# Performance work log

Hardware: AMD Instinct MI355X
Metric: run time of the kernel (lower is better)

The kernel has to match this reference:

```python
import jax, jax.numpy as jnp
import numpy as np

B, T, D, H = 4, 2048, 1024, 16


def setup_inputs() -> dict:
    key = jax.random.key(0)
    ks = jax.random.split(key, 5)
    s = 0.02  # keep activations sane
    return {
        "x": jax.random.normal(ks[0], (B, T, D), jnp.float32),
        "Wq": jax.random.normal(ks[1], (D, D), jnp.float32) * s,
        "bq": jnp.zeros((D,), jnp.float32),
        "Wk": jax.random.normal(ks[2], (D, D), jnp.float32) * s,
        "bk": jnp.zeros((D,), jnp.float32),
        "Wv": jax.random.normal(ks[3], (D, D), jnp.float32) * s,
        "bv": jnp.zeros((D,), jnp.float32),
        "Wo": jax.random.normal(ks[4], (D, D), jnp.float32) * s,
        "bo": jnp.zeros((D,), jnp.float32),
    }


def _split_heads(t):  # (B,T,D) -> (B,H,T,d)
    b, s, d = t.shape
    return t.reshape(b, s, H, d // H).transpose(0, 2, 1, 3)


def reference(x, Wq, bq, Wk, bk, Wv, bv, Wo, bo):
    d_k = D // H
    q = _split_heads(x @ Wq + bq)  # (B,H,T,d)
    k = _split_heads(x @ Wk + bk)
    v = _split_heads(x @ Wv + bv)
    # scaled dot-product similarities (B,H,T,T)
    scores = jnp.einsum("bhqd,bhkd->bhqk", q, k) / jnp.sqrt(jnp.asarray(d_k, x.dtype))
    # causal mask: masked_fill(tril==0, -inf)
    causal = jnp.tril(jnp.ones((T, T), bool))
    scores = jnp.where(causal, scores, -jnp.inf)
    attn = jax.nn.softmax(scores, axis=-1)
    ctx = jnp.einsum("bhqk,bhkd->bhqd", attn, v)  # (B,H,T,d)
    ctx = ctx.transpose(0, 2, 1, 3).reshape(x.shape[0], T, D)
    return ctx @ Wo + bo
```

## Files before the change

### kernel.cpp

```cpp
#include <hip/hip_runtime.h>
#include <hip/hip_bf16.h>

typedef unsigned short u16;
typedef __attribute__((ext_vector_type(8))) short bf16x8;
typedef __attribute__((ext_vector_type(4))) short bf16x4;
typedef __attribute__((ext_vector_type(4))) float f32x4;

#define DD 1024
#define TT 2048
#define HH 16
#define BB 4
#define DK 64
#define MM 8192

#define QSCALE 0.180336880f

__device__ __forceinline__ u16 f2b(float x) {
  __hip_bfloat16 h = __float2bfloat16(x);
  return *reinterpret_cast<u16*>(&h);
}

__device__ __forceinline__ unsigned pk2(float a, float b) {
  float2 t; t.x = a; t.y = b;
  __hip_bfloat162 h = __float22bfloat162_rn(t);
  union { __hip_bfloat162 h; unsigned u; } cv;
  cv.h = h;
  return cv.u;
}

#define GLD16(gp, lp)                                                         \
  __builtin_amdgcn_global_load_lds(                                           \
      (const __attribute__((address_space(1))) unsigned int*)(gp),            \
      (__attribute__((address_space(3))) unsigned int*)(lp), 16, 0, 0)

__global__ __launch_bounds__(256) void cast_bf16_kernel(
    const float* __restrict__ src, u16* __restrict__ dst, int n) {
  int i = (blockIdx.x * 256 + threadIdx.x) * 4;
  if (i + 3 < n) {
    float4 v = *reinterpret_cast<const float4*>(src + i);
    ushort4 o;
    o.x = f2b(v.x); o.y = f2b(v.y); o.z = f2b(v.z); o.w = f2b(v.w);
    *reinterpret_cast<ushort4*>(dst + i) = o;
  }
}

__global__ __launch_bounds__(256) void transpose_cast_kernel(
    const float* __restrict__ W0, const float* __restrict__ W1,
    const float* __restrict__ W2, const float* __restrict__ W3,
    u16* __restrict__ O0, u16* __restrict__ O1,
    u16* __restrict__ O2, u16* __restrict__ O3) {
  const float* W; u16* O;
  switch (blockIdx.z) {
    case 0: W = W0; O = O0; break;
    case 1: W = W1; O = O1; break;
    case 2: W = W2; O = O2; break;
    default: W = W3; O = O3; break;
  }
  __shared__ float tile[32][33];
  int tx = threadIdx.x, ty = threadIdx.y;
  int bx = blockIdx.x * 32;
  int by = blockIdx.y * 32;
#pragma unroll
  for (int j = 0; j < 4; j++)
    tile[ty + j * 8][tx] = W[(size_t)(by + ty + j * 8) * DD + bx + tx];
  __syncthreads();
#pragma unroll
  for (int j = 0; j < 4; j++)
    O[(size_t)(bx + ty + j * 8) * DD + by + tx] = f2b(tile[tx][ty + j * 8]);
}

#define GEMM_STAGE(Aptr, Bptr, Asl, Bsl)                                      \
  _Pragma("unroll") for (int c = 0; c < 4; c++) {                             \
    int idx = tid * 8 + c * 2048;                                             \
    int row = idx >> 6, ck = idx & 63;                                        \
    int src = ck ^ ((row & 7) << 3);                                          \
    GLD16(Aptr + (size_t)(m0 + row) * DD + k0 + src, Asl + idx);              \
    GLD16(Bptr + (size_t)(n0 + row) * DD + k0 + src, Bsl + idx);              \
  }

#define GEMM_MFMA(Asl, Bsl)                                                   \
  _Pragma("unroll") for (int half = 0; half < 2; half++) {                    \
    bf16x8 af[4], bfr[4];                                                     \
    _Pragma("unroll") for (int mb = 0; mb < 4; mb++) {                        \
      int r = wm + mb * 16 + l16;                                             \
      af[mb] = *reinterpret_cast<const bf16x8*>(                              \
          &Asl[r * 64 + ((half * 32 + quad * 8) ^ ((r & 7) << 3))]);          \
    }                                                                         \
    _Pragma("unroll") for (int nb = 0; nb < 4; nb++) {                        \
      int r = wn + nb * 16 + l16;                                             \
      bfr[nb] = *reinterpret_cast<const bf16x8*>(                             \
          &Bsl[r * 64 + ((half * 32 + quad * 8) ^ ((r & 7) << 3))]);          \
    }                                                                         \
    _Pragma("unroll") for (int mb = 0; mb < 4; mb++)                          \
      _Pragma("unroll") for (int nb = 0; nb < 4; nb++)                        \
          acc[mb][nb] = __builtin_amdgcn_mfma_f32_16x16x32_bf16(              \
              af[mb], bfr[nb], acc[mb][nb], 0, 0, 0);                         \
  }

__global__ __launch_bounds__(256, 4) void gemm_qkv_kernel(
    const u16* __restrict__ A,
    const u16* __restrict__ WtQ, const u16* __restrict__ WtK,
    const u16* __restrict__ WtV,
    const float* __restrict__ bq, const float* __restrict__ bk,
    const float* __restrict__ bv,
    u16* __restrict__ Qo, u16* __restrict__ Ko, u16* __restrict__ Vo) {
  __shared__ __align__(16) u16 smem[17408];
  u16* As = smem;
  u16* Bs = smem + 8192;
  u16* Vs = smem;
  int z = blockIdx.z;
  const u16* Bt = (z == 0) ? WtQ : ((z == 1) ? WtK : WtV);
  const float* bias = (z == 0) ? bq : ((z == 1) ? bk : bv);
  int tid = threadIdx.x;
  int wave = tid >> 6, lane = tid & 63;
  int quad = lane >> 4, l16 = lane & 15;
  int m0 = blockIdx.x * 128, n0 = blockIdx.y * 128;
  int wm = (wave >> 1) * 64, wn = (wave & 1) * 64;

  f32x4 acc[4][4];
#pragma unroll
  for (int i = 0; i < 4; i++)
#pragma unroll
    for (int j = 0; j < 4; j++) acc[i][j] = (f32x4){0.f, 0.f, 0.f, 0.f};

  for (int k0 = 0; k0 < DD; k0 += 64) {
    GEMM_STAGE(A, Bt, As, Bs)
    __syncthreads();
    GEMM_MFMA(As, Bs)
    __syncthreads();
  }

  if (z == 2) {
#pragma unroll
    for (int mb = 0; mb < 4; mb++)
#pragma unroll
      for (int nb = 0; nb < 4; nb++) {
        int col = wn + nb * 16 + l16;
        float bv2 = bias[n0 + col];
#pragma unroll
        for (int r = 0; r < 4; r++) {
          int row = wm + mb * 16 + quad * 4 + r;
          Vs[col * 136 + row] = f2b(acc[mb][nb][r] + bv2);
        }
      }
    __syncthreads();
    int b = m0 >> 11;
    int tloc = m0 & 2047;
#pragma unroll
    for (int i = 0; i < 8; i++) {
      int idx = tid * 8 + i * 2048;
      int row = idx >> 7, col = idx & 127;
      uint4 v = *reinterpret_cast<const uint4*>(&Vs[row * 136 + col]);
      int ncol = n0 + row, h = ncol >> 6, dd = ncol & 63;
      *reinterpret_cast<uint4*>(
          Vo + (((size_t)(b * HH + h) * DK) + dd) * TT + tloc + col) = v;
    }
    return;
  }

  u16* outp = (z == 0) ? Qo : Ko;
  float scale = (z == 0) ? QSCALE : 1.0f;
#pragma unroll
  for (int mb = 0; mb < 4; mb++) {
#pragma unroll
    for (int nb = 0; nb < 4; nb++) {
      int col = n0 + wn + nb * 16 + l16;
      float bv2 = bias[col];
#pragma unroll
      for (int r = 0; r < 4; r++) {
        int row = m0 + wm + mb * 16 + quad * 4 + r;
        float val = (acc[mb][nb][r] + bv2) * scale;
        int hh = col >> 6, dd = col & 63;
        int b = row >> 11, t = row & 2047;
        outp[(((size_t)(b * HH + hh) * TT) + t) * DK + dd] = f2b(val);
      }
    }
  }
}

__global__ __launch_bounds__(256, 4) void gemm_out_kernel(
    const u16* __restrict__ A, const u16* __restrict__ Bt,
    const float* __restrict__ bias, float* __restrict__ outp) {
  __shared__ __align__(16) u16 As[128 * 64];
  __shared__ __align__(16) u16 Bs[128 * 64];
  int tid = threadIdx.x;
  int wave = tid >> 6, lane = tid & 63;
  int quad = lane >> 4, l16 = lane & 15;
  int m0 = blockIdx.x * 128, n0 = blockIdx.y * 128;
  int wm = (wave >> 1) * 64, wn = (wave & 1) * 64;

  f32x4 acc[4][4];
#pragma unroll
  for (int i = 0; i < 4; i++)
#pragma unroll
    for (int j = 0; j < 4; j++) acc[i][j] = (f32x4){0.f, 0.f, 0.f, 0.f};

  for (int k0 = 0; k0 < DD; k0 += 64) {
    GEMM_STAGE(A, Bt, As, Bs)
    __syncthreads();
    GEMM_MFMA(As, Bs)
    __syncthreads();
  }

#pragma unroll
  for (int mb = 0; mb < 4; mb++) {
#pragma unroll
    for (int nb = 0; nb < 4; nb++) {
      int col = n0 + wn + nb * 16 + l16;
      float bv = bias[col];
#pragma unroll
      for (int r = 0; r < 4; r++) {
        int row = m0 + wm + mb * 16 + quad * 4 + r;
        outp[(size_t)row * DD + col] = acc[mb][nb][r] + bv;
      }
    }
  }
}

__global__ __launch_bounds__(512, 4) void attn_kernel(
    const u16* __restrict__ Q, const u16* __restrict__ K,
    const u16* __restrict__ VT, u16* __restrict__ ctx) {
  __shared__ __align__(16) u16 Ks[2][64][72];
  __shared__ __align__(16) u16 Vt[2][64][72];

  int tid = threadIdx.x;
  int wave = tid >> 6, lane = tid & 63;
  int quad = lane >> 4, l16 = lane & 15;
  int bid = blockIdx.x;
  int bh = bid & 63;
  int px = bid >> 6;
  int qt = px < 4 ? 15 - px : (px < 8 ? px + 4 : (px < 12 ? px - 4 : 15 - px));
  int b = bh >> 4, h = bh & 15;
  const u16* Qh = Q + (size_t)bh * TT * DK;
  const u16* Kh = K + (size_t)bh * TT * DK;
  const u16* Vh = VT + (size_t)bh * DK * TT;
  int sidx = tid * 8;

  int ktmax = 2 * qt + 1;
  int dtile = 2 * qt + (wave >> 2);
  int qrl = (wave * 16 + l16) & 63;

  const u16* qrow = Qh + (size_t)(qt * 128 + wave * 16 + l16) * DK + quad * 8;
  bf16x8 qf0 = *reinterpret_cast<const bf16x8*>(qrow);
  bf16x8 qf1 = *reinterpret_cast<const bf16x8*>(qrow + 32);

  uint4 kpre = *reinterpret_cast<const uint4*>(Kh + sidx);
  uint4 vpre = *reinterpret_cast<const uint4*>(Vh + (size_t)(sidx >> 6) * TT + (sidx & 63));
  *reinterpret_cast<uint4*>(&Ks[0][sidx >> 6][sidx & 63]) = kpre;
  *reinterpret_cast<uint4*>(&Vt[0][sidx >> 6][sidx & 63]) = vpre;
  __syncthreads();

  f32x4 oacc[4];
#pragma unroll
  for (int dt = 0; dt < 4; dt++) oacc[dt] = (f32x4){0.f, 0.f, 0.f, 0.f};
  f32x4 lacc = (f32x4){0.f, 0.f, 0.f, 0.f};
  const bf16x4 ones = (bf16x4){0x3F80, 0x3F80, 0x3F80, 0x3F80};

  for (int kt = 0; kt <= ktmax; kt++) {
    int cur = kt & 1, nxt = cur ^ 1;
    bool more = kt < ktmax;
    if (more) {
      kpre = *reinterpret_cast<const uint4*>(Kh + (size_t)(kt + 1) * 4096 + sidx);
      vpre = *reinterpret_cast<const uint4*>(
          Vh + (size_t)(sidx >> 6) * TT + (kt + 1) * 64 + (sidx & 63));
    }

    if (kt <= dtile) {
      f32x4 sacc[4];
#pragma unroll
      for (int kb = 0; kb < 4; kb++) sacc[kb] = (f32x4){0.f, 0.f, 0.f, 0.f};
#pragma unroll
      for (int kb = 0; kb < 4; kb++) {
        bf16x8 kf0 = *reinterpret_cast<const bf16x8*>(&Ks[cur][kb * 16 + l16][quad * 8]);
        bf16x8 kf1 = *reinterpret_cast<const bf16x8*>(&Ks[cur][kb * 16 + l16][32 + quad * 8]);
        sacc[kb] = __builtin_amdgcn_mfma_f32_16x16x32_bf16(kf0, qf0, sacc[kb], 0, 0, 0);
        sacc[kb] = __builtin_amdgcn_mfma_f32_16x16x32_bf16(kf1, qf1, sacc[kb], 0, 0, 0);
      }

      if (kt == dtile) {
#pragma unroll
        for (int kb = 0; kb < 4; kb++)
#pragma unroll
          for (int r = 0; r < 4; r++)
            if (kb * 16 + quad * 4 + r > qrl) sacc[kb][r] = -__builtin_inff();
      }

#pragma unroll
      for (int kb = 0; kb < 4; kb++) {
        float p0 = __builtin_amdgcn_exp2f(sacc[kb][0]);
        float p1 = __builtin_amdgcn_exp2f(sacc[kb][1]);
        float p2 = __builtin_amdgcn_exp2f(sacc[kb][2]);
        float p3 = __builtin_amdgcn_exp2f(sacc[kb][3]);
        union { unsigned u[2]; bf16x4 v; } pk;
        pk.u[0] = pk2(p0, p1);
        pk.u[1] = pk2(p2, p3);
        lacc = __builtin_amdgcn_mfma_f32_16x16x16bf16_1k(pk.v, ones, lacc, 0, 0, 0);
#pragma unroll
        for (int dt = 0; dt < 4; dt++) {
          bf16x4 vf = *reinterpret_cast<const bf16x4*>(
              &Vt[cur][dt * 16 + l16][kb * 16 + quad * 4]);
          oacc[dt] = __builtin_amdgcn_mfma_f32_16x16x16bf16_1k(pk.v, vf, oacc[dt], 0, 0, 0);
        }
      }
    }

    if (more) {
      *reinterpret_cast<uint4*>(&Ks[nxt][sidx >> 6][sidx & 63]) = kpre;
      *reinterpret_cast<uint4*>(&Vt[nxt][sidx >> 6][sidx & 63]) = vpre;
    }
    __syncthreads();
  }

  f32x4 inv;
#pragma unroll
  for (int r = 0; r < 4; r++) inv[r] = 1.0f / lacc[r];

  u16* Obuf = &Ks[0][0][0];
#pragma unroll
  for (int dt = 0; dt < 4; dt++)
#pragma unroll
    for (int r = 0; r < 4; r++)
      Obuf[(wave * 16 + quad * 4 + r) * 72 + dt * 16 + l16] =
          f2b(oacc[dt][r] * inv[r]);
  asm volatile("s_waitcnt lgkmcnt(0)" ::: "memory");
#pragma unroll
  for (int i = 0; i < 2; i++) {
    int idx = lane * 8 + i * 512;
    int row = idx >> 6, colc = idx & 63;
    uint4 v = *reinterpret_cast<const uint4*>(&Obuf[(wave * 16 + row) * 72 + colc]);
    int t = qt * 128 + wave * 16 + row;
    *reinterpret_cast<uint4*>(
        ctx + ((size_t)(b * TT + t)) * DD + h * DK + colc) = v;
  }
}

extern "C" void kernel_launch(void* const* d_in, const int* in_sizes, int n_in,
                              void* d_out, int out_size, void* d_ws, size_t ws_size,
                              hipStream_t stream) {
  const float* x  = (const float*)d_in[0];
  const float* Wq = (const float*)d_in[1];
  const float* bq = (const float*)d_in[2];
  const float* Wk = (const float*)d_in[3];
  const float* bk = (const float*)d_in[4];
  const float* Wv = (const float*)d_in[5];
  const float* bv = (const float*)d_in[6];
  const float* Wo = (const float*)d_in[7];
  const float* bo = (const float*)d_in[8];
  float* out = (float*)d_out;

  char* ws = (char*)d_ws;
  size_t off = 0;
  u16* xb  = (u16*)(ws + off); off += (size_t)MM * DD * 2;
  u16* wtq = (u16*)(ws + off); off += (size_t)DD * DD * 2;
  u16* wtk = (u16*)(ws + off); off += (size_t)DD * DD * 2;
  u16* wtv = (u16*)(ws + off); off += (size_t)DD * DD * 2;
  u16* wto = (u16*)(ws + off); off += (size_t)DD * DD * 2;
  u16* Qb  = (u16*)(ws + off); off += (size_t)MM * DD * 2;
  u16* Kb  = (u16*)(ws + off); off += (size_t)MM * DD * 2;
  u16* VTb = (u16*)(ws + off); off += (size_t)MM * DD * 2;
  u16* ctx = (u16*)(ws + off); off += (size_t)MM * DD * 2;

  {
    int n = MM * DD;
    cast_bf16_kernel<<<n / 1024, 256, 0, stream>>>(x, xb, n);
  }
  {
    dim3 grid(DD / 32, DD / 32, 4);
    dim3 block(32, 8);
    transpose_cast_kernel<<<grid, block, 0, stream>>>(Wq, Wk, Wv, Wo, wtq, wtk, wtv, wto);
  }
  {
    dim3 grid(MM / 128, DD / 128, 3);
    gemm_qkv_kernel<<<grid, 256, 0, stream>>>(xb, wtq, wtk, wtv, bq, bk, bv,
                                              Qb, Kb, VTb);
  }
  {
    attn_kernel<<<1024, 512, 0, stream>>>(Qb, Kb, VTb, ctx);
  }
  {
    dim3 grid(MM / 128, DD / 128);
    gemm_out_kernel<<<grid, 256, 0, stream>>>(ctx, wto, bo, out);
  }
}
```

Before: 237.9 us.

## Pair causal query tiles per block and widen key tiles to 128

The attention kernel now launches 512 blocks, each processing two query tiles (15-px and px) in sequence so every block does a balanced amount of causal work. Key/value tiles grow from 64 to 128 keys per iteration, halving the number of barriers and loads per query tile. On the diagonal tile each wave skips key sub-blocks above its own rows instead of computing and masking them. LDS use doubles per block and the sequential phases reduce parallelism, which may lower occupancy and latency hiding.

```diff
diff --git a/kernel.cpp b/kernel.cpp
--- a/kernel.cpp
+++ b/kernel.cpp
@@ -220,8 +220,8 @@
 __global__ __launch_bounds__(512, 4) void attn_kernel(
     const u16* __restrict__ Q, const u16* __restrict__ K,
     const u16* __restrict__ VT, u16* __restrict__ ctx) {
-  __shared__ __align__(16) u16 Ks[2][64][72];
-  __shared__ __align__(16) u16 Vt[2][64][72];
+  __shared__ __align__(16) u16 Ks[2][128][72];
+  __shared__ __align__(16) u16 Vt[2][64][136];
 
   int tid = threadIdx.x;
   int wave = tid >> 6, lane = tid & 63;
@@ -229,68 +229,67 @@
   int bid = blockIdx.x;
   int bh = bid & 63;
   int px = bid >> 6;
-  int qt = px < 4 ? 15 - px : (px < 8 ? px + 4 : (px < 12 ? px - 4 : 15 - px));
   int b = bh >> 4, h = bh & 15;
   const u16* Qh = Q + (size_t)bh * TT * DK;
   const u16* Kh = K + (size_t)bh * TT * DK;
   const u16* Vh = VT + (size_t)bh * DK * TT;
-  int sidx = tid * 8;
-
-  int ktmax = 2 * qt + 1;
-  int dtile = 2 * qt + (wave >> 2);
-  int qrl = (wave * 16 + l16) & 63;
-
-  const u16* qrow = Qh + (size_t)(qt * 128 + wave * 16 + l16) * DK + quad * 8;
-  bf16x8 qf0 = *reinterpret_cast<const bf16x8*>(qrow);
-  bf16x8 qf1 = *reinterpret_cast<const bf16x8*>(qrow + 32);
-
-  uint4 kpre = *reinterpret_cast<const uint4*>(Kh + sidx);
-  uint4 vpre = *reinterpret_cast<const uint4*>(Vh + (size_t)(sidx >> 6) * TT + (sidx & 63));
-  *reinterpret_cast<uint4*>(&Ks[0][sidx >> 6][sidx & 63]) = kpre;
-  *reinterpret_cast<uint4*>(&Vt[0][sidx >> 6][sidx & 63]) = vpre;
-  __syncthreads();
-
-  f32x4 oacc[4];
-#pragma unroll
-  for (int dt = 0; dt < 4; dt++) oacc[dt] = (f32x4){0.f, 0.f, 0.f, 0.f};
-  f32x4 lacc = (f32x4){0.f, 0.f, 0.f, 0.f};
+
+  int ki0 = tid * 8, ki1 = tid * 8 + 4096;
   const bf16x4 ones = (bf16x4){0x3F80, 0x3F80, 0x3F80, 0x3F80};
 
-  for (int kt = 0; kt <= ktmax; kt++) {
-    int cur = kt & 1, nxt = cur ^ 1;
-    bool more = kt < ktmax;
-    if (more) {
-      kpre = *reinterpret_cast<const uint4*>(Kh + (size_t)(kt + 1) * 4096 + sidx);
-      vpre = *reinterpret_cast<const uint4*>(
-          Vh + (size_t)(sidx >> 6) * TT + (kt + 1) * 64 + (sidx & 63));
-    }
-
-    if (kt <= dtile) {
-      f32x4 sacc[4];
-#pragma unroll
-      for (int kb = 0; kb < 4; kb++) sacc[kb] = (f32x4){0.f, 0.f, 0.f, 0.f};
-#pragma unroll
-      for (int kb = 0; kb < 4; kb++) {
+  for (int phase = 0; phase < 2; phase++) {
+    int qtc = phase ? px : (15 - px);
+    __syncthreads();
+
+    const u16* qrow = Qh + (size_t)(qtc * 128 + wave * 16 + l16) * DK + quad * 8;
+    bf16x8 qf0 = *reinterpret_cast<const bf16x8*>(qrow);
+    bf16x8 qf1 = *reinterpret_cast<const bf16x8*>(qrow + 32);
+
+    uint4 kp0 = *reinterpret_cast<const uint4*>(Kh + ki0);
+    uint4 kp1 = *reinterpret_cast<const uint4*>(Kh + ki1);
+    uint4 vp0 = *reinterpret_cast<const uint4*>(Vh + (size_t)(ki0 >> 7) * TT + (ki0 & 127));
+    uint4 vp1 = *reinterpret_cast<const uint4*>(Vh + (size_t)(ki1 >> 7) * TT + (ki1 & 127));
+    *reinterpret_cast<uint4*>(&Ks[0][ki0 >> 6][ki0 & 63]) = kp0;
+    *reinterpret_cast<uint4*>(&Ks[0][ki1 >> 6][ki1 & 63]) = kp1;
+    *reinterpret_cast<uint4*>(&Vt[0][ki0 >> 7][ki0 & 127]) = vp0;
+    *reinterpret_cast<uint4*>(&Vt[0][ki1 >> 7][ki1 & 127]) = vp1;
+    __syncthreads();
+
+    f32x4 oacc[4];
+#pragma unroll
+    for (int dt = 0; dt < 4; dt++) oacc[dt] = (f32x4){0.f, 0.f, 0.f, 0.f};
+    f32x4 lacc = (f32x4){0.f, 0.f, 0.f, 0.f};
+
+    for (int kt = 0; kt <= qtc; kt++) {
+      int cur = kt & 1, nxt = cur ^ 1;
+      bool more = kt < qtc;
+      bool diag = kt == qtc;
+      if (more) {
+        kp0 = *reinterpret_cast<const uint4*>(Kh + (size_t)(kt + 1) * 8192 + ki0);
+        kp1 = *reinterpret_cast<const uint4*>(Kh + (size_t)(kt + 1) * 8192 + ki1);
+        vp0 = *reinterpret_cast<const uint4*>(
+            Vh + (size_t)(ki0 >> 7) * TT + (kt + 1) * 128 + (ki0 & 127));
+        vp1 = *reinterpret_cast<const uint4*>(
+            Vh + (size_t)(ki1 >> 7) * TT + (kt + 1) * 128 + (ki1 & 127));
+      }
+
+#pragma unroll
+      for (int kb = 0; kb < 8; kb++) {
+        if (diag && kb > wave) continue;
         bf16x8 kf0 = *reinterpret_cast<const bf16x8*>(&Ks[cur][kb * 16 + l16][quad * 8]);
         bf16x8 kf1 = *reinterpret_cast<const bf16x8*>(&Ks[cur][kb * 16 + l16][32 + quad * 8]);
-        sacc[kb] = __builtin_amdgcn_mfma_f32_16x16x32_bf16(kf0, qf0, sacc[kb], 0, 0, 0);
-        sacc[kb] = __builtin_amdgcn_mfma_f32_16x16x32_bf16(kf1, qf1, sacc[kb], 0, 0, 0);
-      }
-
-      if (kt == dtile) {
-#pragma unroll
-        for (int kb = 0; kb < 4; kb++)
+        f32x4 sacc = (f32x4){0.f, 0.f, 0.f, 0.f};
+        sacc = __builtin_amdgcn_mfma_f32_16x16x32_bf16(kf0, qf0, sacc, 0, 0, 0);
+        sacc = __builtin_amdgcn_mfma_f32_16x16x32_bf16(kf1, qf1, sacc, 0, 0, 0);
+        if (diag && kb == wave) {
 #pragma unroll
           for (int r = 0; r < 4; r++)
-            if (kb * 16 + quad * 4 + r > qrl) sacc[kb][r] = -__builtin_inff();
-      }
-
-#pragma unroll
-      for (int kb = 0; kb < 4; kb++) {
-        float p0 = __builtin_amdgcn_exp2f(sacc[kb][0]);
-        float p1 = __builtin_amdgcn_exp2f(sacc[kb][1]);
-        float p2 = __builtin_amdgcn_exp2f(sacc[kb][2]);
-        float p3 = __builtin_amdgcn_exp2f(sacc[kb][3]);
+            if (quad * 4 + r > l16) sacc[r] = -__builtin_inff();
+        }
+        float p0 = __builtin_amdgcn_exp2f(sacc[0]);
+        float p1 = __builtin_amdgcn_exp2f(sacc[1]);
+        float p2 = __builtin_amdgcn_exp2f(sacc[2]);
+        float p3 = __builtin_amdgcn_exp2f(sacc[3]);
         union { unsigned u[2]; bf16x4 v; } pk;
         pk.u[0] = pk2(p0, p1);
         pk.u[1] = pk2(p2, p3);
@@ -302,35 +301,37 @@
           oacc[dt] = __builtin_amdgcn_mfma_f32_16x16x16bf16_1k(pk.v, vf, oacc[dt], 0, 0, 0);
         }
       }
-    }
-
-    if (more) {
-      *reinterpret_cast<uint4*>(&Ks[nxt][sidx >> 6][sidx & 63]) = kpre;
-      *reinterpret_cast<uint4*>(&Vt[nxt][sidx >> 6][sidx & 63]) = vpre;
-    }
-    __syncthreads();
-  }
-
-  f32x4 inv;
-#pragma unroll
-  for (int r = 0; r < 4; r++) inv[r] = 1.0f / lacc[r];
-
-  u16* Obuf = &Ks[0][0][0];
-#pragma unroll
-  for (int dt = 0; dt < 4; dt++)
-#pragma unroll
-    for (int r = 0; r < 4; r++)
-      Obuf[(wave * 16 + quad * 4 + r) * 72 + dt * 16 + l16] =
-          f2b(oacc[dt][r] * inv[r]);
-  asm volatile("s_waitcnt lgkmcnt(0)" ::: "memory");
-#pragma unroll
-  for (int i = 0; i < 2; i++) {
-    int idx = lane * 8 + i * 512;
-    int row = idx >> 6, colc = idx & 63;
-    uint4 v = *reinterpret_cast<const uint4*>(&Obuf[(wave * 16 + row) * 72 + colc]);
-    int t = qt * 128 + wave * 16 + row;
-    *reinterpret_cast<uint4*>(
-        ctx + ((size_t)(b * TT + t)) * DD + h * DK + colc) = v;
+
+      if (more) {
+        *reinterpret_cast<uint4*>(&Ks[nxt][ki0 >> 6][ki0 & 63]) = kp0;
+        *reinterpret_cast<uint4*>(&Ks[nxt][ki1 >> 6][ki1 & 63]) = kp1;
+        *reinterpret_cast<uint4*>(&Vt[nxt][ki0 >> 7][ki0 & 127]) = vp0;
+        *reinterpret_cast<uint4*>(&Vt[nxt][ki1 >> 7][ki1 & 127]) = vp1;
+      }
+      __syncthreads();
+    }
+
+    f32x4 inv;
+#pragma unroll
+    for (int r = 0; r < 4; r++) inv[r] = 1.0f / lacc[r];
+
+    u16* Obuf = &Ks[0][0][0];
+#pragma unroll
+    for (int dt = 0; dt < 4; dt++)
+#pragma unroll
+      for (int r = 0; r < 4; r++)
+        Obuf[(wave * 16 + quad * 4 + r) * 72 + dt * 16 + l16] =
+            f2b(oacc[dt][r] * inv[r]);
+    asm volatile("s_waitcnt lgkmcnt(0)" ::: "memory");
+#pragma unroll
+    for (int i = 0; i < 2; i++) {
+      int idx = lane * 8 + i * 512;
+      int row = idx >> 6, colc = idx & 63;
+      uint4 v = *reinterpret_cast<const uint4*>(&Obuf[(wave * 16 + row) * 72 + colc]);
+      int t = qtc * 128 + wave * 16 + row;
+      *reinterpret_cast<uint4*>(
+          ctx + ((size_t)(b * TT + t)) * DD + h * DK + colc) = v;
+    }
   }
 }
 
@@ -375,7 +376,7 @@
                                               Qb, Kb, VTb);
   }
   {
-    attn_kernel<<<1024, 512, 0, stream>>>(Qb, Kb, VTb, ctx);
+    attn_kernel<<<512, 512, 0, stream>>>(Qb, Kb, VTb, ctx);
   }
   {
     dim3 grid(MM / 128, DD / 128);
```

New measurement: 236.7 us. Within noise of the previous version (-0.5%).
